# Kernel tuning notes

Measured on AMD Instinct MI355X. Metric: run time of the kernel, lower is better.

The kernel has to match this reference:

```python
import jax, jax.numpy as jnp
import numpy as np

B, N, D, K, H = 32768, 17, 2, 3, 64


def _mlp_params(key, n, d_in, d_hid, d_out):
    k1, k2, k3, k4 = jax.random.split(key, 4)
    W1 = jax.random.normal(k1, (n, d_in, d_hid), jnp.float32) / np.sqrt(d_in)
    b1 = jnp.zeros((n, d_hid), jnp.float32)
    W2 = jax.random.normal(k2, (n, d_hid, d_out), jnp.float32) / np.sqrt(d_hid)
    b2 = jnp.zeros((n, d_out), jnp.float32)
    return W1, b1, W2, b2


def setup_inputs() -> dict:
    key = jax.random.key(0)
    kp, kk, kw, kb = jax.random.split(key, 4)
    pred_pts = jax.random.normal(kp, (B, N, D), jnp.float32)
    kW1, kb1, kW2, kb2 = _mlp_params(kk, N, D, H, K)            # k_nets
    wW1, wb1, wW2, wb2 = _mlp_params(kw, N, D, H, K)            # weight_nets
    bW1, bb1, bW2, bb2 = _mlp_params(kb, N, D, 2 * H, K * 2 * D)  # basis_nets
    return dict(pred_pts=pred_pts,
                kW1=kW1, kb1=kb1, kW2=kW2, kb2=kb2,
                wW1=wW1, wb1=wb1, wW2=wW2, wb2=wb2,
                bW1=bW1, bb1=bb1, bW2=bW2, bb2=bb2)


def _per_joint_mlp(x, W1, b1, W2, b2):
    # x: [B,N,D]; W1: [N,D,Hd]; W2: [N,Hd,O]
    h = jax.nn.relu(jnp.einsum('bnd,ndh->bnh', x, W1) + b1[None])
    return jnp.einsum('bnh,nho->bno', h, W2) + b2[None]


def reference(pred_pts, kW1, kb1, kW2, kb2, wW1, wb1, wW2, wb2, bW1, bb1, bW2, bb2):
    Bc, Nc, Dc = pred_pts.shape
    Kc = kW2.shape[-1]

    # k-selection head (eval mode: argmax, +1)
    k_logits = _per_joint_mlp(pred_pts, kW1, kb1, kW2, kb2)      # [B,N,K]
    k_js = jnp.argmax(k_logits, axis=-1) + 1                     # [B,N] int

    # mixture weights
    w = jax.nn.softmax(_per_joint_mlp(pred_pts, wW1, wb1, wW2, wb2), axis=-1)  # [B,N,K]

    # basis parameters: mu, sigma = exp(log_sigma)
    params = _per_joint_mlp(pred_pts, bW1, bb1, bW2, bb2).reshape(Bc, Nc, Kc, 2 * Dc)
    mu = params[..., :Dc]                                         # [B,N,K,D]
    sigma = jnp.exp(params[..., Dc:])                             # [B,N,K,D]

    # top-k selection by descending weight (indices are constants w.r.t. grad)
    idx = jnp.argsort(-w, axis=-1)                                # [B,N,K]
    mu_top = jnp.take_along_axis(mu, idx[..., None], axis=2)      # [B,N,K,D]
    sigma_top = jnp.take_along_axis(sigma, idx[..., None], axis=2)
    mask = jnp.arange(Kc)[None, None, :] < k_js[..., None]        # [B,N,K] bool

    # pack float outputs: weights + selected (mu, sigma) -> [B,N,K,1+2D]
    out = jnp.concatenate([w[..., None], mu_top, sigma_top], axis=-1)
    return out, k_js, mask
```

## Files before the change

kernel.cpp:

```cpp
#include <hip/hip_runtime.h>
#include <cmath>

#define NBATCH 32768
#define NJOINT 17
#define OUT0_ELEMS (NBATCH * NJOINT * 15)
#define KJS_OFF    OUT0_ELEMS
#define MASK_OFF   (KJS_OFF + NBATCH * NJOINT)

__device__ __forceinline__ float sel3f(int i, float a, float b, float c) {
    return (i == 0) ? a : ((i == 1) ? b : c);
}

__global__ __launch_bounds__(256) void mdn_fused(
    const float* __restrict__ pred_pts,
    const float* __restrict__ kW1, const float* __restrict__ kb1,
    const float* __restrict__ kW2, const float* __restrict__ kb2,
    const float* __restrict__ wW1, const float* __restrict__ wb1,
    const float* __restrict__ wW2, const float* __restrict__ wb2,
    const float* __restrict__ bW1, const float* __restrict__ bb1,
    const float* __restrict__ bW2, const float* __restrict__ bb2,
    float* __restrict__ out)
{
    const int n = blockIdx.y;
    const int b = blockIdx.x * 256 + threadIdx.x;
    const int p = b * NJOINT + n;

    const float2 xv = *reinterpret_cast<const float2*>(pred_pts + 2 * p);
    const float x0f = xv.x, x1f = xv.y;
    const double x0 = (double)x0f, x1 = (double)x1f;

    double kl0, kl1, kl2;
    {
        const float* W1a = kW1 + n * 128;
        const float* W1b = W1a + 64;
        const float* b1  = kb1 + n * 64;
        const float* W2  = kW2 + n * 192;
        kl0 = (double)kb2[n * 3 + 0];
        kl1 = (double)kb2[n * 3 + 1];
        kl2 = (double)kb2[n * 3 + 2];
        #pragma unroll 8
        for (int h = 0; h < 64; ++h) {
            double hv = fma(x1, (double)W1b[h], fma(x0, (double)W1a[h], (double)b1[h]));
            hv = fmax(hv, 0.0);
            kl0 = fma(hv, (double)W2[h * 3 + 0], kl0);
            kl1 = fma(hv, (double)W2[h * 3 + 1], kl1);
            kl2 = fma(hv, (double)W2[h * 3 + 2], kl2);
        }
    }
    int kj = 0;
    {
        double m = kl0;
        if (kl1 > m) { m = kl1; kj = 1; }
        if (kl2 > m) { kj = 2; }
    }

    double wl0, wl1, wl2;
    {
        const float* W1a = wW1 + n * 128;
        const float* W1b = W1a + 64;
        const float* b1  = wb1 + n * 64;
        const float* W2  = wW2 + n * 192;
        wl0 = (double)wb2[n * 3 + 0];
        wl1 = (double)wb2[n * 3 + 1];
        wl2 = (double)wb2[n * 3 + 2];
        #pragma unroll 8
        for (int h = 0; h < 64; ++h) {
            double hv = fma(x1, (double)W1b[h], fma(x0, (double)W1a[h], (double)b1[h]));
            hv = fmax(hv, 0.0);
            wl0 = fma(hv, (double)W2[h * 3 + 0], wl0);
            wl1 = fma(hv, (double)W2[h * 3 + 1], wl1);
            wl2 = fma(hv, (double)W2[h * 3 + 2], wl2);
        }
    }
    int i0 = 0;
    {
        double m = wl0;
        if (wl1 > m) { m = wl1; i0 = 1; }
        if (wl2 > m) { i0 = 2; }
    }
    const int ia = (i0 == 0) ? 1 : 0;
    const int ib = (i0 == 2) ? 1 : 2;
    const double wa = ia ? wl1 : wl0;
    const double wb = (ib == 1) ? wl1 : wl2;
    const int i1 = (wb > wa) ? ib : ia;
    const int i2 = (wb > wa) ? ia : ib;

    const double mw = fmax(fmax(wl0, wl1), wl2);
    const float e0 = __expf((float)(wl0 - mw));
    const float e1 = __expf((float)(wl1 - mw));
    const float e2 = __expf((float)(wl2 - mw));
    const float inv = 1.0f / (e0 + e1 + e2);
    const float p0 = e0 * inv, p1 = e1 * inv, p2 = e2 * inv;

    float acc[12];
    {
        const float* W1a = bW1 + n * 256;
        const float* W1b = W1a + 128;
        const float* b1  = bb1 + n * 128;
        const float* W2  = bW2 + n * 1536;
        const float* b2  = bb2 + n * 12;
        #pragma unroll
        for (int j = 0; j < 12; ++j) acc[j] = b2[j];
        #pragma unroll 4
        for (int h = 0; h < 128; ++h) {
            float hv = fmaxf(fmaf(x1f, W1b[h], fmaf(x0f, W1a[h], b1[h])), 0.0f);
            #pragma unroll
            for (int j = 0; j < 12; ++j)
                acc[j] = fmaf(hv, W2[h * 12 + j], acc[j]);
        }
    }

    float r[15];
    r[0]  = p0; r[5] = p1; r[10] = p2;

    r[1]  = sel3f(i0, acc[0], acc[4], acc[8]);
    r[2]  = sel3f(i0, acc[1], acc[5], acc[9]);
    r[3]  = __expf(sel3f(i0, acc[2], acc[6], acc[10]));
    r[4]  = __expf(sel3f(i0, acc[3], acc[7], acc[11]));

    r[6]  = sel3f(i1, acc[0], acc[4], acc[8]);
    r[7]  = sel3f(i1, acc[1], acc[5], acc[9]);
    r[8]  = __expf(sel3f(i1, acc[2], acc[6], acc[10]));
    r[9]  = __expf(sel3f(i1, acc[3], acc[7], acc[11]));

    r[11] = sel3f(i2, acc[0], acc[4], acc[8]);
    r[12] = sel3f(i2, acc[1], acc[5], acc[9]);
    r[13] = __expf(sel3f(i2, acc[2], acc[6], acc[10]));
    r[14] = __expf(sel3f(i2, acc[3], acc[7], acc[11]));

    float* o = out + (size_t)p * 15;
    #pragma unroll
    for (int i = 0; i < 15; ++i) o[i] = r[i];

    out[KJS_OFF + p] = (float)(kj + 1);

    float* mk = out + MASK_OFF + (size_t)p * 3;
    mk[0] = 1.0f;
    mk[1] = (kj >= 1) ? 1.0f : 0.0f;
    mk[2] = (kj >= 2) ? 1.0f : 0.0f;
}

extern "C" void kernel_launch(void* const* d_in, const int* in_sizes, int n_in,
                              void* d_out, int out_size, void* d_ws, size_t ws_size,
                              hipStream_t stream) {
    (void)in_sizes; (void)n_in; (void)d_ws; (void)ws_size; (void)out_size;
    dim3 grid(NBATCH / 256, NJOINT);
    mdn_fused<<<grid, 256, 0, stream>>>(
        (const float*)d_in[0],
        (const float*)d_in[1], (const float*)d_in[2],
        (const float*)d_in[3], (const float*)d_in[4],
        (const float*)d_in[5], (const float*)d_in[6],
        (const float*)d_in[7], (const float*)d_in[8],
        (const float*)d_in[9], (const float*)d_in[10],
        (const float*)d_in[11], (const float*)d_in[12],
        (float*)d_out);
}
```

Before: 149.1 us.

## Remap waves to joints, stage outputs in LDS, pre-convert weights to f64

Each block now holds 64 batch rows across 4 joints, with one wavefront per joint. The joint index is made wave-uniform via readfirstlane, so weight loads can become scalar. Outputs are staged in shared memory and written back so that consecutive joints of the same batch row land contiguously, which coalesces the strided 15-float per-point stores. A small pre-kernel converts the k/w MLP weights to double in the workspace to drop per-thread float-to-double conversions. This adds an extra launch, a __syncthreads, and a last joint group that is only partly filled.

```diff
diff --git a/kernel.cpp b/kernel.cpp
--- a/kernel.cpp
+++ b/kernel.cpp
@@ -7,10 +7,180 @@
 #define KJS_OFF    OUT0_ELEMS
 #define MASK_OFF   (KJS_OFF + NBATCH * NJOINT)
 
+#define WN_STRIDE 774
+#define WS_DOUBLES (NJOINT * WN_STRIDE)
+
 __device__ __forceinline__ float sel3f(int i, float a, float b, float c) {
     return (i == 0) ? a : ((i == 1) ? b : c);
 }
 
+__global__ void cvt_weights_f64(
+    const float* __restrict__ kW1, const float* __restrict__ kb1,
+    const float* __restrict__ kW2, const float* __restrict__ kb2,
+    const float* __restrict__ wW1, const float* __restrict__ wb1,
+    const float* __restrict__ wW2, const float* __restrict__ wb2,
+    double* __restrict__ dws)
+{
+    const int n = blockIdx.x;
+    double* o = dws + (size_t)n * WN_STRIDE;
+    for (int i = threadIdx.x; i < WN_STRIDE; i += blockDim.x) {
+        int j = i;
+        const float* W1 = kW1; const float* b1 = kb1;
+        const float* W2 = kW2; const float* b2 = kb2;
+        if (j >= 387) { j -= 387; W1 = wW1; b1 = wb1; W2 = wW2; b2 = wb2; }
+        float v;
+        if (j < 128)      v = W1[n * 128 + j];
+        else if (j < 192) v = b1[n * 64 + (j - 128)];
+        else if (j < 384) v = W2[n * 192 + (j - 192)];
+        else              v = b2[n * 3 + (j - 384)];
+        o[i] = (double)v;
+    }
+}
+
+template<bool USE_WS>
+__device__ __forceinline__ void compute_point(
+    int n, float x0f, float x1f,
+    const float* __restrict__ kW1, const float* __restrict__ kb1,
+    const float* __restrict__ kW2, const float* __restrict__ kb2,
+    const float* __restrict__ wW1, const float* __restrict__ wb1,
+    const float* __restrict__ wW2, const float* __restrict__ wb2,
+    const float* __restrict__ bW1, const float* __restrict__ bb1,
+    const float* __restrict__ bW2, const float* __restrict__ bb2,
+    const double* __restrict__ dws,
+    float r[15], int& kj_out)
+{
+    const double x0 = (double)x0f, x1 = (double)x1f;
+    double kl0, kl1, kl2, wl0, wl1, wl2;
+
+    if constexpr (USE_WS) {
+        const double* Wn = dws + (size_t)n * WN_STRIDE;
+        {
+            const double* W1a = Wn;
+            const double* W1b = Wn + 64;
+            const double* b1  = Wn + 128;
+            const double* W2  = Wn + 192;
+            kl0 = Wn[384]; kl1 = Wn[385]; kl2 = Wn[386];
+            #pragma unroll 4
+            for (int h = 0; h < 64; ++h) {
+                double hv = fmax(fma(x1, W1b[h], fma(x0, W1a[h], b1[h])), 0.0);
+                kl0 = fma(hv, W2[h * 3 + 0], kl0);
+                kl1 = fma(hv, W2[h * 3 + 1], kl1);
+                kl2 = fma(hv, W2[h * 3 + 2], kl2);
+            }
+        }
+        {
+            const double* W1a = Wn + 387;
+            const double* W1b = Wn + 451;
+            const double* b1  = Wn + 515;
+            const double* W2  = Wn + 579;
+            wl0 = Wn[771]; wl1 = Wn[772]; wl2 = Wn[773];
+            #pragma unroll 4
+            for (int h = 0; h < 64; ++h) {
+                double hv = fmax(fma(x1, W1b[h], fma(x0, W1a[h], b1[h])), 0.0);
+                wl0 = fma(hv, W2[h * 3 + 0], wl0);
+                wl1 = fma(hv, W2[h * 3 + 1], wl1);
+                wl2 = fma(hv, W2[h * 3 + 2], wl2);
+            }
+        }
+    } else {
+        {
+            const float* W1a = kW1 + n * 128;
+            const float* W1b = W1a + 64;
+            const float* b1  = kb1 + n * 64;
+            const float* W2  = kW2 + n * 192;
+            kl0 = (double)kb2[n * 3 + 0];
+            kl1 = (double)kb2[n * 3 + 1];
+            kl2 = (double)kb2[n * 3 + 2];
+            #pragma unroll 4
+            for (int h = 0; h < 64; ++h) {
+                double hv = fma(x1, (double)W1b[h], fma(x0, (double)W1a[h], (double)b1[h]));
+                hv = fmax(hv, 0.0);
+                kl0 = fma(hv, (double)W2[h * 3 + 0], kl0);
+                kl1 = fma(hv, (double)W2[h * 3 + 1], kl1);
+                kl2 = fma(hv, (double)W2[h * 3 + 2], kl2);
+            }
+        }
+        {
+            const float* W1a = wW1 + n * 128;
+            const float* W1b = W1a + 64;
+            const float* b1  = wb1 + n * 64;
+            const float* W2  = wW2 + n * 192;
+            wl0 = (double)wb2[n * 3 + 0];
+            wl1 = (double)wb2[n * 3 + 1];
+            wl2 = (double)wb2[n * 3 + 2];
+            #pragma unroll 4
+            for (int h = 0; h < 64; ++h) {
+                double hv = fma(x1, (double)W1b[h], fma(x0, (double)W1a[h], (double)b1[h]));
+                hv = fmax(hv, 0.0);
+                wl0 = fma(hv, (double)W2[h * 3 + 0], wl0);
+                wl1 = fma(hv, (double)W2[h * 3 + 1], wl1);
+                wl2 = fma(hv, (double)W2[h * 3 + 2], wl2);
+            }
+        }
+    }
+
+    int kj = 0;
+    {
+        double m = kl0;
+        if (kl1 > m) { m = kl1; kj = 1; }
+        if (kl2 > m) { kj = 2; }
+    }
+    kj_out = kj;
+
+    int i0 = 0;
+    {
+        double m = wl0;
+        if (wl1 > m) { m = wl1; i0 = 1; }
+        if (wl2 > m) { i0 = 2; }
+    }
+    const int ia = (i0 == 0) ? 1 : 0;
+    const int ib = (i0 == 2) ? 1 : 2;
+    const double wa = ia ? wl1 : wl0;
+    const double wb = (ib == 1) ? wl1 : wl2;
+    const int i1 = (wb > wa) ? ib : ia;
+    const int i2 = (wb > wa) ? ia : ib;
+
+    const double mw = fmax(fmax(wl0, wl1), wl2);
+    const float e0 = __expf((float)(wl0 - mw));
+    const float e1 = __expf((float)(wl1 - mw));
+    const float e2 = __expf((float)(wl2 - mw));
+    const float inv = 1.0f / (e0 + e1 + e2);
+    const float p0 = e0 * inv, p1 = e1 * inv, p2 = e2 * inv;
+
+    float acc[12];
+    {
+        const float* W1a = bW1 + n * 256;
+        const float* W1b = W1a + 128;
+        const float* b1  = bb1 + n * 128;
+        const float* W2  = bW2 + n * 1536;
+        const float* b2  = bb2 + n * 12;
+        #pragma unroll
+        for (int j = 0; j < 12; ++j) acc[j] = b2[j];
+        #pragma unroll 4
+        for (int h = 0; h < 128; ++h) {
+            float hv = fmaxf(fmaf(x1f, W1b[h], fmaf(x0f, W1a[h], b1[h])), 0.0f);
+            #pragma unroll
+            for (int j = 0; j < 12; ++j)
+                acc[j] = fmaf(hv, W2[h * 12 + j], acc[j]);
+        }
+    }
+
+    r[0]  = p0; r[5] = p1; r[10] = p2;
+    r[1]  = sel3f(i0, acc[0], acc[4], acc[8]);
+    r[2]  = sel3f(i0, acc[1], acc[5], acc[9]);
+    r[3]  = __expf(sel3f(i0, acc[2], acc[6], acc[10]));
+    r[4]  = __expf(sel3f(i0, acc[3], acc[7], acc[11]));
+    r[6]  = sel3f(i1, acc[0], acc[4], acc[8]);
+    r[7]  = sel3f(i1, acc[1], acc[5], acc[9]);
+    r[8]  = __expf(sel3f(i1, acc[2], acc[6], acc[10]));
+    r[9]  = __expf(sel3f(i1, acc[3], acc[7], acc[11]));
+    r[11] = sel3f(i2, acc[0], acc[4], acc[8]);
+    r[12] = sel3f(i2, acc[1], acc[5], acc[9]);
+    r[13] = __expf(sel3f(i2, acc[2], acc[6], acc[10]));
+    r[14] = __expf(sel3f(i2, acc[3], acc[7], acc[11]));
+}
+
+template<bool USE_WS>
 __global__ __launch_bounds__(256) void mdn_fused(
     const float* __restrict__ pred_pts,
     const float* __restrict__ kW1, const float* __restrict__ kb1,
@@ -19,139 +189,110 @@
     const float* __restrict__ wW2, const float* __restrict__ wb2,
     const float* __restrict__ bW1, const float* __restrict__ bb1,
     const float* __restrict__ bW2, const float* __restrict__ bb2,
-    float* __restrict__ out)
+    float* __restrict__ out,
+    const double* __restrict__ dws)
 {
-    const int n = blockIdx.y;
-    const int b = blockIdx.x * 256 + threadIdx.x;
+    const int l    = threadIdx.x;
+    const int w    = l >> 6;
+    const int lane = l & 63;
+    const int bx   = blockIdx.x;
+    const int by   = blockIdx.y;
+    const int n0   = by * 4;
+
+    int n = n0 + w;
+    if (n >= NJOINT) return;
+    n = __builtin_amdgcn_readfirstlane(n);
+
+    const int b = bx * 64 + lane;
     const int p = b * NJOINT + n;
 
     const float2 xv = *reinterpret_cast<const float2*>(pred_pts + 2 * p);
-    const float x0f = xv.x, x1f = xv.y;
-    const double x0 = (double)x0f, x1 = (double)x1f;
-
-    double kl0, kl1, kl2;
-    {
-        const float* W1a = kW1 + n * 128;
-        const float* W1b = W1a + 64;
-        const float* b1  = kb1 + n * 64;
-        const float* W2  = kW2 + n * 192;
-        kl0 = (double)kb2[n * 3 + 0];
-        kl1 = (double)kb2[n * 3 + 1];
-        kl2 = (double)kb2[n * 3 + 2];
-        #pragma unroll 8
-        for (int h = 0; h < 64; ++h) {
-            double hv = fma(x1, (double)W1b[h], fma(x0, (double)W1a[h], (double)b1[h]));
-            hv = fmax(hv, 0.0);
-            kl0 = fma(hv, (double)W2[h * 3 + 0], kl0);
-            kl1 = fma(hv, (double)W2[h * 3 + 1], kl1);
-            kl2 = fma(hv, (double)W2[h * 3 + 2], kl2);
-        }
-    }
-    int kj = 0;
-    {
-        double m = kl0;
-        if (kl1 > m) { m = kl1; kj = 1; }
-        if (kl2 > m) { kj = 2; }
-    }
-
-    double wl0, wl1, wl2;
-    {
-        const float* W1a = wW1 + n * 128;
-        const float* W1b = W1a + 64;
-        const float* b1  = wb1 + n * 64;
-        const float* W2  = wW2 + n * 192;
-        wl0 = (double)wb2[n * 3 + 0];
-        wl1 = (double)wb2[n * 3 + 1];
-        wl2 = (double)wb2[n * 3 + 2];
-        #pragma unroll 8
-        for (int h = 0; h < 64; ++h) {
-            double hv = fma(x1, (double)W1b[h], fma(x0, (double)W1a[h], (double)b1[h]));
-            hv = fmax(hv, 0.0);
-            wl0 = fma(hv, (double)W2[h * 3 + 0], wl0);
-            wl1 = fma(hv, (double)W2[h * 3 + 1], wl1);
-            wl2 = fma(hv, (double)W2[h * 3 + 2], wl2);
-        }
-    }
-    int i0 = 0;
-    {
-        double m = wl0;
-        if (wl1 > m) { m = wl1; i0 = 1; }
-        if (wl2 > m) { i0 = 2; }
-    }
-    const int ia = (i0 == 0) ? 1 : 0;
-    const int ib = (i0 == 2) ? 1 : 2;
-    const double wa = ia ? wl1 : wl0;
-    const double wb = (ib == 1) ? wl1 : wl2;
-    const int i1 = (wb > wa) ? ib : ia;
-    const int i2 = (wb > wa) ? ia : ib;
-
-    const double mw = fmax(fmax(wl0, wl1), wl2);
-    const float e0 = __expf((float)(wl0 - mw));
-    const float e1 = __expf((float)(wl1 - mw));
-    const float e2 = __expf((float)(wl2 - mw));
-    const float inv = 1.0f / (e0 + e1 + e2);
-    const float p0 = e0 * inv, p1 = e1 * inv, p2 = e2 * inv;
-
-    float acc[12];
-    {
-        const float* W1a = bW1 + n * 256;
-        const float* W1b = W1a + 128;
-        const float* b1  = bb1 + n * 128;
-        const float* W2  = bW2 + n * 1536;
-        const float* b2  = bb2 + n * 12;
-        #pragma unroll
-        for (int j = 0; j < 12; ++j) acc[j] = b2[j];
-        #pragma unroll 4
-        for (int h = 0; h < 128; ++h) {
-            float hv = fmaxf(fmaf(x1f, W1b[h], fmaf(x0f, W1a[h], b1[h])), 0.0f);
-            #pragma unroll
-            for (int j = 0; j < 12; ++j)
-                acc[j] = fmaf(hv, W2[h * 12 + j], acc[j]);
-        }
-    }
 
     float r[15];
-    r[0]  = p0; r[5] = p1; r[10] = p2;
-
-    r[1]  = sel3f(i0, acc[0], acc[4], acc[8]);
-    r[2]  = sel3f(i0, acc[1], acc[5], acc[9]);
-    r[3]  = __expf(sel3f(i0, acc[2], acc[6], acc[10]));
-    r[4]  = __expf(sel3f(i0, acc[3], acc[7], acc[11]));
-
-    r[6]  = sel3f(i1, acc[0], acc[4], acc[8]);
-    r[7]  = sel3f(i1, acc[1], acc[5], acc[9]);
-    r[8]  = __expf(sel3f(i1, acc[2], acc[6], acc[10]));
-    r[9]  = __expf(sel3f(i1, acc[3], acc[7], acc[11]));
-
-    r[11] = sel3f(i2, acc[0], acc[4], acc[8]);
-    r[12] = sel3f(i2, acc[1], acc[5], acc[9]);
-    r[13] = __expf(sel3f(i2, acc[2], acc[6], acc[10]));
-    r[14] = __expf(sel3f(i2, acc[3], acc[7], acc[11]));
-
-    float* o = out + (size_t)p * 15;
-    #pragma unroll
-    for (int i = 0; i < 15; ++i) o[i] = r[i];
-
-    out[KJS_OFF + p] = (float)(kj + 1);
-
-    float* mk = out + MASK_OFF + (size_t)p * 3;
-    mk[0] = 1.0f;
-    mk[1] = (kj >= 1) ? 1.0f : 0.0f;
-    mk[2] = (kj >= 2) ? 1.0f : 0.0f;
+    int kj;
+    compute_point<USE_WS>(n, xv.x, xv.y,
+                          kW1, kb1, kW2, kb2, wW1, wb1, wW2, wb2,
+                          bW1, bb1, bW2, bb2, dws, r, kj);
+
+    if (by == 4) {
+        float* o = out + (size_t)p * 15;
+        #pragma unroll
+        for (int i = 0; i < 15; ++i) o[i] = r[i];
+        out[KJS_OFF + p] = (float)(kj + 1);
+        float* mk = out + MASK_OFF + (size_t)p * 3;
+        mk[0] = 1.0f;
+        mk[1] = (kj >= 1) ? 1.0f : 0.0f;
+        mk[2] = (kj >= 2) ? 1.0f : 0.0f;
+        return;
+    }
+
+    __shared__ float s_out[256 * 17];
+    {
+        float* so = s_out + (w * 64 + lane) * 17;
+        #pragma unroll
+        for (int j = 0; j < 15; ++j) so[j] = r[j];
+        so[15] = (float)(kj + 1);
+    }
+    __syncthreads();
+
+    if (l < 240) {
+        const int c_off = l / 60;
+        const int jj    = l - c_off * 60;
+        const int nl    = jj / 15;
+        const int j     = jj - nl * 15;
+        const int lbase = nl * 1088 + c_off * 17 + j;
+        size_t g = (size_t)((bx * 64 + c_off) * NJOINT + n0) * 15 + jj;
+        #pragma unroll
+        for (int rr = 0; rr < 16; ++rr) {
+            out[g] = s_out[lbase + 68 * rr];
+            g += 1020;
+        }
+    }
+
+    {
+        const int bl  = l >> 2;
+        const int nlr = l & 3;
+        const float kjf = s_out[(nlr * 64 + bl) * 17 + 15];
+        const int pg = (bx * 64 + bl) * NJOINT + n0 + nlr;
+        out[KJS_OFF + pg] = kjf;
+        float* mk = out + MASK_OFF + (size_t)pg * 3;
+        mk[0] = 1.0f;
+        mk[1] = (kjf >= 1.5f) ? 1.0f : 0.0f;
+        mk[2] = (kjf >= 2.5f) ? 1.0f : 0.0f;
+    }
 }
 
 extern "C" void kernel_launch(void* const* d_in, const int* in_sizes, int n_in,
                               void* d_out, int out_size, void* d_ws, size_t ws_size,
                               hipStream_t stream) {
-    (void)in_sizes; (void)n_in; (void)d_ws; (void)ws_size; (void)out_size;
-    dim3 grid(NBATCH / 256, NJOINT);
-    mdn_fused<<<grid, 256, 0, stream>>>(
-        (const float*)d_in[0],
-        (const float*)d_in[1], (const float*)d_in[2],
-        (const float*)d_in[3], (const float*)d_in[4],
-        (const float*)d_in[5], (const float*)d_in[6],
-        (const float*)d_in[7], (const float*)d_in[8],
-        (const float*)d_in[9], (const float*)d_in[10],
-        (const float*)d_in[11], (const float*)d_in[12],
-        (float*)d_out);
-}
+    (void)in_sizes; (void)n_in; (void)out_size;
+    const bool use_ws = (d_ws != nullptr) && (ws_size >= (size_t)WS_DOUBLES * sizeof(double));
+    dim3 grid(NBATCH / 64, 5);
+    if (use_ws) {
+        cvt_weights_f64<<<NJOINT, 256, 0, stream>>>(
+            (const float*)d_in[1], (const float*)d_in[2],
+            (const float*)d_in[3], (const float*)d_in[4],
+            (const float*)d_in[5], (const float*)d_in[6],
+            (const float*)d_in[7], (const float*)d_in[8],
+            (double*)d_ws);
+        mdn_fused<true><<<grid, 256, 0, stream>>>(
+            (const float*)d_in[0],
+            (const float*)d_in[1], (const float*)d_in[2],
+            (const float*)d_in[3], (const float*)d_in[4],
+            (const float*)d_in[5], (const float*)d_in[6],
+            (const float*)d_in[7], (const float*)d_in[8],
+            (const float*)d_in[9], (const float*)d_in[10],
+            (const float*)d_in[11], (const float*)d_in[12],
+            (float*)d_out, (const double*)d_ws);
+    } else {
+        mdn_fused<false><<<grid, 256, 0, stream>>>(
+            (const float*)d_in[0],
+            (const float*)d_in[1], (const float*)d_in[2],
+            (const float*)d_in[3], (const float*)d_in[4],
+            (const float*)d_in[5], (const float*)d_in[6],
+            (const float*)d_in[7], (const float*)d_in[8],
+            (const float*)d_in[9], (const float*)d_in[10],
+            (const float*)d_in[11], (const float*)d_in[12],
+            (float*)d_out, nullptr);
+    }
+}
```

Result: faster. 145.6 us (-2.3%).

## Stage per-joint weights in LDS and coalesce output stores via shared-memory transpose

Applied to the files above, without the earlier changes.

Each block now handles two joints for 128 batch rows. It first loads both joints' MLP weights into LDS, packing the k/w nets as pre-converted doubles and the basis net as interleaved float groups, so every hidden unit's weights sit together. Results are then staged in LDS and written back as contiguous spans covering both adjacent joints, replacing the old stride-17 per-point writes. This is meant to cut scattered global weight loads and poorly coalesced output stores, at the cost of more LDS, extra barriers and a special case for the last, odd joint.

```diff
diff --git a/kernel.cpp b/kernel.cpp
--- a/kernel.cpp
+++ b/kernel.cpp
@@ -7,11 +7,100 @@
 #define KJS_OFF    OUT0_ELEMS
 #define MASK_OFF   (KJS_OFF + NBATCH * NJOINT)
 
+#define KW_DBL   774
+#define BW_FLT   2064
+#define NBYTES_KW (KW_DBL * 8)
+#define NBYTES_N  (NBYTES_KW + BW_FLT * 4)
+#define TILE_B   128
+#define SMEM_BYTES (2 * NBYTES_N)
+
 __device__ __forceinline__ float sel3f(int i, float a, float b, float c) {
     return (i == 0) ? a : ((i == 1) ? b : c);
 }
 
-__global__ __launch_bounds__(256) void mdn_fused(
+__device__ __forceinline__ void compute_point_lds(
+    const char* __restrict__ wbase, float x0f, float x1f,
+    float r[15], int& kj_out)
+{
+    const double x0 = (double)x0f, x1 = (double)x1f;
+    const double* kw = (const double*)wbase;
+    const float*  bw = (const float*)(wbase + NBYTES_KW);
+
+    double kl0 = kw[768], kl1 = kw[769], kl2 = kw[770];
+    #pragma unroll 4
+    for (int h = 0; h < 64; ++h) {
+        const double* g = kw + h * 6;
+        double hv = fmax(fma(x1, g[1], fma(x0, g[0], g[2])), 0.0);
+        kl0 = fma(hv, g[3], kl0);
+        kl1 = fma(hv, g[4], kl1);
+        kl2 = fma(hv, g[5], kl2);
+    }
+    double wl0 = kw[771], wl1 = kw[772], wl2 = kw[773];
+    #pragma unroll 4
+    for (int h = 0; h < 64; ++h) {
+        const double* g = kw + 384 + h * 6;
+        double hv = fmax(fma(x1, g[1], fma(x0, g[0], g[2])), 0.0);
+        wl0 = fma(hv, g[3], wl0);
+        wl1 = fma(hv, g[4], wl1);
+        wl2 = fma(hv, g[5], wl2);
+    }
+
+    int kj = 0;
+    {
+        double m = kl0;
+        if (kl1 > m) { m = kl1; kj = 1; }
+        if (kl2 > m) { kj = 2; }
+    }
+    kj_out = kj;
+
+    int i0 = 0;
+    {
+        double m = wl0;
+        if (wl1 > m) { m = wl1; i0 = 1; }
+        if (wl2 > m) { i0 = 2; }
+    }
+    const int ia = (i0 == 0) ? 1 : 0;
+    const int ib = (i0 == 2) ? 1 : 2;
+    const double wa = ia ? wl1 : wl0;
+    const double wb = (ib == 1) ? wl1 : wl2;
+    const int i1 = (wb > wa) ? ib : ia;
+    const int i2 = (wb > wa) ? ia : ib;
+
+    const double mw = fmax(fmax(wl0, wl1), wl2);
+    const float e0 = __expf((float)(wl0 - mw));
+    const float e1 = __expf((float)(wl1 - mw));
+    const float e2 = __expf((float)(wl2 - mw));
+    const float inv = 1.0f / (e0 + e1 + e2);
+    const float p0 = e0 * inv, p1 = e1 * inv, p2 = e2 * inv;
+
+    float acc[12];
+    #pragma unroll
+    for (int j = 0; j < 12; ++j) acc[j] = bw[2048 + j];
+    #pragma unroll 4
+    for (int h = 0; h < 128; ++h) {
+        const float* g = bw + h * 16;
+        float hv = fmaxf(fmaf(x1f, g[1], fmaf(x0f, g[0], g[2])), 0.0f);
+        #pragma unroll
+        for (int j = 0; j < 12; ++j)
+            acc[j] = fmaf(hv, g[4 + j], acc[j]);
+    }
+
+    r[0]  = p0; r[5] = p1; r[10] = p2;
+    r[1]  = sel3f(i0, acc[0], acc[4], acc[8]);
+    r[2]  = sel3f(i0, acc[1], acc[5], acc[9]);
+    r[3]  = __expf(sel3f(i0, acc[2], acc[6], acc[10]));
+    r[4]  = __expf(sel3f(i0, acc[3], acc[7], acc[11]));
+    r[6]  = sel3f(i1, acc[0], acc[4], acc[8]);
+    r[7]  = sel3f(i1, acc[1], acc[5], acc[9]);
+    r[8]  = __expf(sel3f(i1, acc[2], acc[6], acc[10]));
+    r[9]  = __expf(sel3f(i1, acc[3], acc[7], acc[11]));
+    r[11] = sel3f(i2, acc[0], acc[4], acc[8]);
+    r[12] = sel3f(i2, acc[1], acc[5], acc[9]);
+    r[13] = __expf(sel3f(i2, acc[2], acc[6], acc[10]));
+    r[14] = __expf(sel3f(i2, acc[3], acc[7], acc[11]));
+}
+
+__global__ __launch_bounds__(256, 4) void mdn_fused(
     const float* __restrict__ pred_pts,
     const float* __restrict__ kW1, const float* __restrict__ kb1,
     const float* __restrict__ kW2, const float* __restrict__ kb2,
@@ -21,130 +110,125 @@
     const float* __restrict__ bW2, const float* __restrict__ bb2,
     float* __restrict__ out)
 {
-    const int n = blockIdx.y;
-    const int b = blockIdx.x * 256 + threadIdx.x;
-    const int p = b * NJOINT + n;
+    __shared__ __align__(16) char smem[SMEM_BYTES];
+
+    const int l    = threadIdx.x;
+    const int w    = l >> 6;
+    const int lane = l & 63;
+    const int bx   = blockIdx.x;
+    const int by   = blockIdx.y;
+    const int n0   = by * 2;
+    const int ncnt = (by == 8) ? 1 : 2;
+
+    for (int e = l; e < ncnt * KW_DBL; e += 256) {
+        const int nsl = (e < KW_DBL) ? 0 : 1;
+        const int j   = e - nsl * KW_DBL;
+        const int n   = n0 + nsl;
+        float f;
+        if (j < 768) {
+            const int g = j / 6, s = j - 6 * g;
+            const int h = g & 63;
+            const bool isw = (g >= 64);
+            const float* W1 = isw ? wW1 : kW1;
+            const float* b1 = isw ? wb1 : kb1;
+            const float* W2 = isw ? wW2 : kW2;
+            f = (s == 0) ? W1[n * 128 + h]
+              : (s == 1) ? W1[n * 128 + 64 + h]
+              : (s == 2) ? b1[n * 64 + h]
+              :            W2[n * 192 + h * 3 + (s - 3)];
+        } else {
+            const int s = j - 768;
+            f = (s < 3) ? kb2[n * 3 + s] : wb2[n * 3 + (s - 3)];
+        }
+        ((double*)(smem + nsl * NBYTES_N))[j] = (double)f;
+    }
+    for (int e = l; e < ncnt * BW_FLT; e += 256) {
+        const int nsl = (e < BW_FLT) ? 0 : 1;
+        const int j   = e - nsl * BW_FLT;
+        const int n   = n0 + nsl;
+        const int g = j >> 4, s = j & 15;
+        float f;
+        if (g < 128) {
+            f = (s == 0) ? bW1[n * 256 + g]
+              : (s == 1) ? bW1[n * 256 + 128 + g]
+              : (s == 2) ? bb1[n * 128 + g]
+              : (s == 3) ? 0.0f
+              :            bW2[n * 1536 + g * 12 + (s - 4)];
+        } else {
+            f = (s < 12) ? bb2[n * 12 + s] : 0.0f;
+        }
+        ((float*)(smem + nsl * NBYTES_N + NBYTES_KW))[j] = f;
+    }
+    __syncthreads();
+
+    if (by == 8 && w >= 2) return;
+
+    const int nsl = __builtin_amdgcn_readfirstlane(w >> 1);
+    const int n   = n0 + nsl;
+    const int bl  = (w & 1) * 64 + lane;
+    const int b   = bx * TILE_B + bl;
+    const int p   = b * NJOINT + n;
 
     const float2 xv = *reinterpret_cast<const float2*>(pred_pts + 2 * p);
-    const float x0f = xv.x, x1f = xv.y;
-    const double x0 = (double)x0f, x1 = (double)x1f;
-
-    double kl0, kl1, kl2;
-    {
-        const float* W1a = kW1 + n * 128;
-        const float* W1b = W1a + 64;
-        const float* b1  = kb1 + n * 64;
-        const float* W2  = kW2 + n * 192;
-        kl0 = (double)kb2[n * 3 + 0];
-        kl1 = (double)kb2[n * 3 + 1];
-        kl2 = (double)kb2[n * 3 + 2];
-        #pragma unroll 8
-        for (int h = 0; h < 64; ++h) {
-            double hv = fma(x1, (double)W1b[h], fma(x0, (double)W1a[h], (double)b1[h]));
-            hv = fmax(hv, 0.0);
-            kl0 = fma(hv, (double)W2[h * 3 + 0], kl0);
-            kl1 = fma(hv, (double)W2[h * 3 + 1], kl1);
-            kl2 = fma(hv, (double)W2[h * 3 + 2], kl2);
+
+    float r[15];
+    int kj;
+    compute_point_lds(smem + nsl * NBYTES_N, xv.x, xv.y, r, kj);
+
+    if (by == 8) {
+        float* o = out + (size_t)p * 15;
+        #pragma unroll
+        for (int i = 0; i < 15; ++i) o[i] = r[i];
+        out[KJS_OFF + p] = (float)(kj + 1);
+        float* mk = out + MASK_OFF + (size_t)p * 3;
+        mk[0] = 1.0f;
+        mk[1] = (kj >= 1) ? 1.0f : 0.0f;
+        mk[2] = (kj >= 2) ? 1.0f : 0.0f;
+        return;
+    }
+
+    float* s_out = (float*)smem;
+    __syncthreads();
+    {
+        float* so = s_out + (nsl * 128 + bl) * 17;
+        #pragma unroll
+        for (int j = 0; j < 15; ++j) so[j] = r[j];
+        so[15] = (float)(kj + 1);
+    }
+    __syncthreads();
+
+    if (l < 240) {
+        const int bgrp = l / 30;
+        const int jj   = l - bgrp * 30;
+        const int nl   = jj / 15;
+        const int j    = jj - nl * 15;
+        const int lbase = (nl * 128 + bgrp) * 17 + j;
+        size_t g = (size_t)((bx * TILE_B + bgrp) * NJOINT + n0) * 15 + jj;
+        #pragma unroll
+        for (int rr = 0; rr < 16; ++rr) {
+            out[g] = s_out[lbase + 136 * rr];
+            g += 2040;
         }
     }
-    int kj = 0;
-    {
-        double m = kl0;
-        if (kl1 > m) { m = kl1; kj = 1; }
-        if (kl2 > m) { kj = 2; }
-    }
-
-    double wl0, wl1, wl2;
-    {
-        const float* W1a = wW1 + n * 128;
-        const float* W1b = W1a + 64;
-        const float* b1  = wb1 + n * 64;
-        const float* W2  = wW2 + n * 192;
-        wl0 = (double)wb2[n * 3 + 0];
-        wl1 = (double)wb2[n * 3 + 1];
-        wl2 = (double)wb2[n * 3 + 2];
-        #pragma unroll 8
-        for (int h = 0; h < 64; ++h) {
-            double hv = fma(x1, (double)W1b[h], fma(x0, (double)W1a[h], (double)b1[h]));
-            hv = fmax(hv, 0.0);
-            wl0 = fma(hv, (double)W2[h * 3 + 0], wl0);
-            wl1 = fma(hv, (double)W2[h * 3 + 1], wl1);
-            wl2 = fma(hv, (double)W2[h * 3 + 2], wl2);
-        }
-    }
-    int i0 = 0;
-    {
-        double m = wl0;
-        if (wl1 > m) { m = wl1; i0 = 1; }
-        if (wl2 > m) { i0 = 2; }
-    }
-    const int ia = (i0 == 0) ? 1 : 0;
-    const int ib = (i0 == 2) ? 1 : 2;
-    const double wa = ia ? wl1 : wl0;
-    const double wb = (ib == 1) ? wl1 : wl2;
-    const int i1 = (wb > wa) ? ib : ia;
-    const int i2 = (wb > wa) ? ia : ib;
-
-    const double mw = fmax(fmax(wl0, wl1), wl2);
-    const float e0 = __expf((float)(wl0 - mw));
-    const float e1 = __expf((float)(wl1 - mw));
-    const float e2 = __expf((float)(wl2 - mw));
-    const float inv = 1.0f / (e0 + e1 + e2);
-    const float p0 = e0 * inv, p1 = e1 * inv, p2 = e2 * inv;
-
-    float acc[12];
-    {
-        const float* W1a = bW1 + n * 256;
-        const float* W1b = W1a + 128;
-        const float* b1  = bb1 + n * 128;
-        const float* W2  = bW2 + n * 1536;
-        const float* b2  = bb2 + n * 12;
-        #pragma unroll
-        for (int j = 0; j < 12; ++j) acc[j] = b2[j];
-        #pragma unroll 4
-        for (int h = 0; h < 128; ++h) {
-            float hv = fmaxf(fmaf(x1f, W1b[h], fmaf(x0f, W1a[h], b1[h])), 0.0f);
-            #pragma unroll
-            for (int j = 0; j < 12; ++j)
-                acc[j] = fmaf(hv, W2[h * 12 + j], acc[j]);
-        }
-    }
-
-    float r[15];
-    r[0]  = p0; r[5] = p1; r[10] = p2;
-
-    r[1]  = sel3f(i0, acc[0], acc[4], acc[8]);
-    r[2]  = sel3f(i0, acc[1], acc[5], acc[9]);
-    r[3]  = __expf(sel3f(i0, acc[2], acc[6], acc[10]));
-    r[4]  = __expf(sel3f(i0, acc[3], acc[7], acc[11]));
-
-    r[6]  = sel3f(i1, acc[0], acc[4], acc[8]);
-    r[7]  = sel3f(i1, acc[1], acc[5], acc[9]);
-    r[8]  = __expf(sel3f(i1, acc[2], acc[6], acc[10]));
-    r[9]  = __expf(sel3f(i1, acc[3], acc[7], acc[11]));
-
-    r[11] = sel3f(i2, acc[0], acc[4], acc[8]);
-    r[12] = sel3f(i2, acc[1], acc[5], acc[9]);
-    r[13] = __expf(sel3f(i2, acc[2], acc[6], acc[10]));
-    r[14] = __expf(sel3f(i2, acc[3], acc[7], acc[11]));
-
-    float* o = out + (size_t)p * 15;
-    #pragma unroll
-    for (int i = 0; i < 15; ++i) o[i] = r[i];
-
-    out[KJS_OFF + p] = (float)(kj + 1);
-
-    float* mk = out + MASK_OFF + (size_t)p * 3;
-    mk[0] = 1.0f;
-    mk[1] = (kj >= 1) ? 1.0f : 0.0f;
-    mk[2] = (kj >= 2) ? 1.0f : 0.0f;
+
+    {
+        const int blr = l >> 1;
+        const int nlr = l & 1;
+        const float kjf = s_out[(nlr * 128 + blr) * 17 + 15];
+        const int pg = (bx * TILE_B + blr) * NJOINT + n0 + nlr;
+        out[KJS_OFF + pg] = kjf;
+        float* mk = out + MASK_OFF + (size_t)pg * 3;
+        mk[0] = 1.0f;
+        mk[1] = (kjf >= 1.5f) ? 1.0f : 0.0f;
+        mk[2] = (kjf >= 2.5f) ? 1.0f : 0.0f;
+    }
 }
 
 extern "C" void kernel_launch(void* const* d_in, const int* in_sizes, int n_in,
                               void* d_out, int out_size, void* d_ws, size_t ws_size,
                               hipStream_t stream) {
     (void)in_sizes; (void)n_in; (void)d_ws; (void)ws_size; (void)out_size;
-    dim3 grid(NBATCH / 256, NJOINT);
+    dim3 grid(NBATCH / TILE_B, 9);
     mdn_fused<<<grid, 256, 0, stream>>>(
         (const float*)d_in[0],
         (const float*)d_in[1], (const float*)d_in[2],
```

Measured after the change: 168.9 us. +13.3%, slower.
